# Kernel tuning notes

Measured on AMD Instinct MI355X. Metric: run time of the kernel, lower is better.

The kernel has to match this reference:

```python
import jax, jax.numpy as jnp
import numpy as np

B, CIN, COUT, H, W = 8, 28, 28, 256, 256
DG, KH, PADH = 7, 7, 3
CPG = CIN // DG  # channels per deformable group


def setup_inputs() -> dict:
    key = jax.random.key(0)
    ks = jax.random.split(key, 6)
    x = jax.random.normal(ks[0], (B, CIN, H, W), jnp.float32)
    weight = jax.random.normal(ks[1], (COUT, CIN, KH, 1), jnp.float32) * 0.02
    bias = jnp.zeros((COUT,), jnp.float32)
    w_t = jax.random.normal(ks[2], (COUT, COUT, 1, 7), jnp.float32) * 0.05
    b_t = jax.random.normal(ks[3], (COUT,), jnp.float32) * 0.05
    w_m = jax.random.normal(ks[4], (DG, DG, 1), jnp.float32) * 0.3
    b_m = jax.random.normal(ks[5], (DG,), jnp.float32) * 0.05
    return {"x": x, "weight": weight, "bias": bias,
            "w_t": w_t, "b_t": b_t, "w_m": w_m, "b_m": b_m}


def _sample_positions(height):
    # Faithful to init_offset: off[g, 2*i, h] = -i + (h+1)/(g+1)*(i+1) - (h+1)
    # x-offset channels stay 0, so sampling only moves along the H (frequency) axis.
    h = jnp.arange(height, dtype=jnp.float32)
    i = jnp.arange(KH, dtype=jnp.float32)
    g = jnp.arange(DG, dtype=jnp.float32)
    off = (-i[None, :, None]
           + (h[None, None, :] + 1.0) / (g[:, None, None] + 1.0) * (i[None, :, None] + 1.0)
           - (h[None, None, :] + 1.0))
    # DCNv2 sample row: h*stride - pad + i*dilation + offset_y
    return h[None, None, :] - PADH + i[None, :, None] + off  # (DG, KH, H)


def reference(x, weight, bias, w_t, b_t, w_m, b_m):
    yp = _sample_positions(H)                       # (DG, KH, H) float sample rows
    y0 = jnp.floor(yp)
    fy = yp - y0                                    # bilinear fraction along H
    y0i = y0.astype(jnp.int32)
    v0ok = ((y0i >= 0) & (y0i <= H - 1)).astype(x.dtype)
    v1ok = ((y0i + 1 >= 0) & (y0i + 1 <= H - 1)).astype(x.dtype)
    y0c = jnp.clip(y0i, 0, H - 1)
    y1c = jnp.clip(y0i + 1, 0, H - 1)

    x_r = x.reshape(B, DG, CPG, H, W)               # offsets grouped over channels
    g_b = jnp.broadcast_to(jnp.arange(DG)[:, None, None], (DG, KH, H))

    def gather(yi):
        v = x_r[:, g_b, :, yi, :]                   # (DG, KH, H, B, CPG, W)
        return jnp.transpose(v, (3, 0, 4, 1, 2, 5))  # (B, DG, CPG, KH, H, W)

    w0 = ((1.0 - fy) * v0ok)[None, :, None, :, :, None]
    w1 = (fy * v1ok)[None, :, None, :, :, None]
    sampled = gather(y0c) * w0 + gather(y1c) * w1   # mask is all-ones in HarmonicConv

    w_r = weight.reshape(COUT, DG, CPG, KH)         # (O, I, 7, 1) -> group view
    out = jnp.einsum('bgcihw,ogci->bohw', sampled, w_r) + bias[None, :, None, None]

    # temporal_conv: Conv2d(C, C, (1,7), pad (0,3))
    out = jax.lax.conv_general_dilated(
        out, w_t, (1, 1), ((0, 0), (3, 3)),
        dimension_numbers=('NCHW', 'OIHW', 'NCHW')) + b_t[None, :, None, None]

    # mixing_conv: Conv1d(7, 7, 1) over reshape (B, 7, C*H*W/7)
    sh = out.shape
    o = out.reshape(B, DG, -1)
    o = jnp.einsum('bgl,fg->bfl', o, w_m[:, :, 0]) + b_m[None, :, None]
    return o.reshape(sh)
```

## Files before the change

### kernel.cpp

```cpp
#include <hip/hip_runtime.h>
#include <hip/hip_bf16.h>

#define B_    8
#define CIN_  28
#define COUT_ 28
#define H_    256
#define W_    256
#define DG_   7
#define KH_   7
#define CPG_  4
#define HW_   (H_*W_)

typedef short short8 __attribute__((ext_vector_type(8)));
typedef short short4v __attribute__((ext_vector_type(4)));
typedef float f32x4 __attribute__((ext_vector_type(4)));

__device__ __forceinline__ short f2bf(float f) {
  __hip_bfloat16 h = __float2bfloat16(f);
  return *reinterpret_cast<short*>(&h);
}

__global__ void prep_weights(const float* __restrict__ weight, const float* __restrict__ bias,
                             const float* __restrict__ w_t, const float* __restrict__ b_t,
                             const float* __restrict__ w_m, const float* __restrict__ b_m,
                             short* __restrict__ A1, short* __restrict__ A2,
                             float* __restrict__ bias32, float* __restrict__ beff32) {
  int idx = blockIdx.x * blockDim.x + threadIdx.x;
  if (idx < 7168) {
    int j = idx & 7;
    int rest = idx >> 3;
    int l = rest & 63;
    int gm = rest >> 6;
    int g = gm % 7, mt = gm / 7;
    int o = mt * 16 + (l & 15);
    int kk = (l >> 4) * 8 + j;
    float v = 0.f;
    if (o < COUT_ && kk < 28) {
      int i = kk >> 2, c = kk & 3;
      v = weight[(o * CIN_ + (g * 4 + c)) * KH_ + i];
    }
    A1[idx] = f2bf(v);
  } else if (idx < 14336) {
    int id = idx - 7168;
    int j = id & 7;
    int rest = id >> 3;
    int l = rest & 63;
    int gm = rest >> 6;
    int ks = gm % 7, mt = gm / 7;
    int o = mt * 16 + (l & 15);
    int kk = (l >> 4) * 8 + j;
    float v = 0.f;
    if (o < COUT_ && kk < 28) {
      int f = o >> 2, cc = o & 3;
#pragma unroll
      for (int g = 0; g < DG_; ++g)
        v += w_m[f * 7 + g] * w_t[((g * 4 + cc) * COUT_ + kk) * 7 + ks];
    }
    A2[id] = f2bf(v);
  }
  if (idx < 32) {
    bias32[idx] = (idx < COUT_) ? bias[idx] : 0.f;
    float s = 0.f;
    if (idx < COUT_) {
      int f = idx >> 2, cc = idx & 3;
      s = b_m[f];
#pragma unroll
      for (int g = 0; g < DG_; ++g) s += w_m[f * 7 + g] * b_t[g * 4 + cc];
    }
    beff32[idx] = s;
  }
}

#define PITCH 40

__global__ __launch_bounds__(256)
void harmonic_mfma(const float* __restrict__ x,
                   const short* __restrict__ A1, const short* __restrict__ A2,
                   const float* __restrict__ bias32, const float* __restrict__ beff32,
                   float* __restrict__ out) {
  __shared__ short Bt[W_ * PITCH];
  __shared__ short Tt[(W_ + 6) * PITCH];

  const int bid = blockIdx.x;
  const int b = bid & 7;
  const int h = bid >> 3;
  const int tid = threadIdx.x;
  const int lane = tid & 63;
  const int wv = tid >> 6;
  const int l15 = lane & 15;
  const int l4 = lane >> 4;
  const int w = tid;

  if (tid < 96) {
    int rsel = tid >> 4;
    int r = (rsel < 3) ? rsel : (256 + rsel);
    ((int*)Tt)[r * (PITCH / 2) + (tid & 15)] = 0;
  }

  f32x4 acc[2][4] = {};
  const float* xb = x + (size_t)b * CIN_ * HW_ + w;

  for (int g = 0; g < DG_; ++g) {
#pragma unroll
    for (int i = 0; i < KH_; ++i) {
      float t   = ((float)(h + 1) / (float)(g + 1)) * (float)(i + 1);
      float off = ((float)(-i) + t) - (float)(h + 1);
      float yp  = (((float)h - 3.0f) + (float)i) + off;
      float y0f = floorf(yp);
      float fy  = yp - y0f;
      int y0i = (int)y0f;
      int y1i = y0i + 1;
      const bool ok0 = (y0i >= 0) && (y0i <= H_ - 1);
      const bool ok1 = (y1i >= 0) && (y1i <= H_ - 1);
      short4v pk = {0, 0, 0, 0};
      if (ok0 || ok1) {
        float a0 = ok0 ? (1.0f - fy) : 0.0f;
        float a1 = ok1 ? fy : 0.0f;
        int y0c = y0i < 0 ? 0 : (y0i > H_ - 1 ? H_ - 1 : y0i);
        int y1c = y1i < 0 ? 0 : (y1i > H_ - 1 ? H_ - 1 : y1i);
        const float* p0 = xb + (size_t)(g * CPG_) * HW_ + y0c * W_;
        const float* p1 = xb + (size_t)(g * CPG_) * HW_ + y1c * W_;
        float v0 = a0 * p0[0 * HW_] + a1 * p1[0 * HW_];
        float v1 = a0 * p0[1 * HW_] + a1 * p1[1 * HW_];
        float v2 = a0 * p0[2 * HW_] + a1 * p1[2 * HW_];
        float v3 = a0 * p0[3 * HW_] + a1 * p1[3 * HW_];
        pk = (short4v){f2bf(v0), f2bf(v1), f2bf(v2), f2bf(v3)};
      }
      *(short4v*)&Bt[w * PITCH + i * 4] = pk;
    }
    if (g == 0) *(short4v*)&Bt[w * PITCH + 28] = (short4v){0, 0, 0, 0};
    __syncthreads();

    short8 a0f = *(const short8*)&A1[((0 * 7 + g) * 64 + lane) * 8];
    short8 a1f = *(const short8*)&A1[((1 * 7 + g) * 64 + lane) * 8];
#pragma unroll
    for (int nt = 0; nt < 4; ++nt) {
      int wcol = wv * 64 + nt * 16 + l15;
      short8 bf = *(const short8*)&Bt[wcol * PITCH + l4 * 8];
      acc[0][nt] = __builtin_amdgcn_mfma_f32_16x16x32_bf16(a0f, bf, acc[0][nt], 0, 0, 0);
      acc[1][nt] = __builtin_amdgcn_mfma_f32_16x16x32_bf16(a1f, bf, acc[1][nt], 0, 0, 0);
    }
    __syncthreads();
  }

#pragma unroll
  for (int mt = 0; mt < 2; ++mt) {
#pragma unroll
    for (int nt = 0; nt < 4; ++nt) {
      int wcol = wv * 64 + nt * 16 + l15;
      int o0 = mt * 16 + l4 * 4;
      f32x4 v = acc[mt][nt];
      short4v pk = {f2bf(v[0] + bias32[o0 + 0]), f2bf(v[1] + bias32[o0 + 1]),
                    f2bf(v[2] + bias32[o0 + 2]), f2bf(v[3] + bias32[o0 + 3])};
      *(short4v*)&Tt[(wcol + 3) * PITCH + o0] = pk;
    }
  }
  __syncthreads();

  f32x4 acc2[2][4] = {};
#pragma unroll
  for (int ks = 0; ks < 7; ++ks) {
    short8 a20 = *(const short8*)&A2[((0 * 7 + ks) * 64 + lane) * 8];
    short8 a21 = *(const short8*)&A2[((1 * 7 + ks) * 64 + lane) * 8];
#pragma unroll
    for (int nt = 0; nt < 4; ++nt) {
      int wcol = wv * 64 + nt * 16 + l15;
      short8 bf = *(const short8*)&Tt[(wcol + ks) * PITCH + l4 * 8];
      acc2[0][nt] = __builtin_amdgcn_mfma_f32_16x16x32_bf16(a20, bf, acc2[0][nt], 0, 0, 0);
      acc2[1][nt] = __builtin_amdgcn_mfma_f32_16x16x32_bf16(a21, bf, acc2[1][nt], 0, 0, 0);
    }
  }

  float* ob = out + (size_t)b * COUT_ * HW_ + h * W_;
#pragma unroll
  for (int mt = 0; mt < 2; ++mt) {
#pragma unroll
    for (int nt = 0; nt < 4; ++nt) {
      int wcol = wv * 64 + nt * 16 + l15;
      int o0 = mt * 16 + l4 * 4;
      f32x4 v = acc2[mt][nt];
#pragma unroll
      for (int q = 0; q < 4; ++q) {
        int o = o0 + q;
        if (o < COUT_) ob[o * HW_ + wcol] = v[q] + beff32[o];
      }
    }
  }
}

extern "C" void kernel_launch(void* const* d_in, const int* in_sizes, int n_in,
                              void* d_out, int out_size, void* d_ws, size_t ws_size,
                              hipStream_t stream) {
  const float* x      = (const float*)d_in[0];
  const float* weight = (const float*)d_in[1];
  const float* bias   = (const float*)d_in[2];
  const float* w_t    = (const float*)d_in[3];
  const float* b_t    = (const float*)d_in[4];
  const float* w_m    = (const float*)d_in[5];
  const float* b_m    = (const float*)d_in[6];
  float* out = (float*)d_out;

  short* A1     = (short*)d_ws;
  short* A2     = A1 + 7168;
  float* bias32 = (float*)(A2 + 7168);
  float* beff32 = bias32 + 32;

  prep_weights<<<56, 256, 0, stream>>>(weight, bias, w_t, b_t, w_m, b_m,
                                       A1, A2, bias32, beff32);
  harmonic_mfma<<<B_ * H_, 256, 0, stream>>>(x, A1, A2, bias32, beff32, out);
}
```

Before: 181.7 us.

## Drop per-group block barriers, precompute tap table, and merge LDS buffers

Each wave now reads back only the LDS columns it wrote itself, so the two __syncthreads per deformable group are removed and the stage-1 tile is synchronised only once. Sample-row indices and bilinear weights are computed once per block into a small per-wave LDS table, instead of being recomputed in the unrolled tap loop. The two staging buffers are merged into one shared array, which roughly halves LDS use and may allow more resident blocks per CU. Stage-1 LDS writes are packed into wider 16-byte stores. The risk is that correctness now depends on wave-local LDS ordering and on reusing the merged buffer safely after the barrier.

```diff
diff --git a/kernel.cpp b/kernel.cpp
--- a/kernel.cpp
+++ b/kernel.cpp
@@ -10,14 +10,23 @@
 #define KH_   7
 #define CPG_  4
 #define HW_   (H_*W_)
-
-typedef short short8 __attribute__((ext_vector_type(8)));
+#define PITCH 40
+#define NTAP  (DG_*KH_)
+
+typedef short short8  __attribute__((ext_vector_type(8)));
 typedef short short4v __attribute__((ext_vector_type(4)));
-typedef float f32x4 __attribute__((ext_vector_type(4)));
+typedef float f32x4   __attribute__((ext_vector_type(4)));
 
 __device__ __forceinline__ short f2bf(float f) {
   __hip_bfloat16 h = __float2bfloat16(f);
   return *reinterpret_cast<short*>(&h);
+}
+
+__device__ __forceinline__ short8 cat8(short4v a, short4v b) {
+  short8 r;
+  r[0]=a[0]; r[1]=a[1]; r[2]=a[2]; r[3]=a[3];
+  r[4]=b[0]; r[5]=b[1]; r[6]=b[2]; r[7]=b[3];
+  return r;
 }
 
 __global__ void prep_weights(const float* __restrict__ weight, const float* __restrict__ bias,
@@ -71,15 +80,13 @@
   }
 }
 
-#define PITCH 40
-
 __global__ __launch_bounds__(256)
 void harmonic_mfma(const float* __restrict__ x,
                    const short* __restrict__ A1, const short* __restrict__ A2,
                    const float* __restrict__ bias32, const float* __restrict__ beff32,
                    float* __restrict__ out) {
-  __shared__ short Bt[W_ * PITCH];
-  __shared__ short Tt[(W_ + 6) * PITCH];
+  __shared__ short S[(W_ + 6) * PITCH];
+  __shared__ float4 yts[4][NTAP];
 
   const int bid = blockIdx.x;
   const int b = bid & 7;
@@ -91,56 +98,73 @@
   const int l4 = lane >> 4;
   const int w = tid;
 
+  if (lane < NTAP) {
+    int g = lane / 7;
+    int i = lane - g * 7;
+    float t   = ((float)(h + 1) / (float)(g + 1)) * (float)(i + 1);
+    float off = ((float)(-i) + t) - (float)(h + 1);
+    float yp  = (((float)h - 3.0f) + (float)i) + off;
+    float y0f = floorf(yp);
+    float fy  = yp - y0f;
+    int y0i = (int)y0f;
+    int y1i = y0i + 1;
+    bool ok0 = (y0i >= 0) && (y0i <= H_ - 1);
+    bool ok1 = (y1i >= 0) && (y1i <= H_ - 1);
+    float a0 = ok0 ? (1.0f - fy) : 0.0f;
+    float a1 = ok1 ? fy : 0.0f;
+    int y0c = y0i < 0 ? 0 : (y0i > H_ - 1 ? H_ - 1 : y0i);
+    int y1c = y1i < 0 ? 0 : (y1i > H_ - 1 ? H_ - 1 : y1i);
+    float4 e;
+    e.x = a0; e.y = a1;
+    e.z = __int_as_float(g * CPG_ * HW_ + y0c * W_);
+    e.w = __int_as_float(g * CPG_ * HW_ + y1c * W_);
+    yts[wv][lane] = e;
+  }
+
+  f32x4 acc[2][4] = {};
+  const float* xb = x + (size_t)b * CIN_ * HW_ + w;
+
+  *(short4v*)&S[w * PITCH + 28] = (short4v){0, 0, 0, 0};
+
+  for (int g = 0; g < DG_; ++g) {
+    short4v pk[KH_];
+#pragma unroll
+    for (int i = 0; i < KH_; ++i) {
+      float4 e = yts[wv][g * 7 + i];
+      short4v p = {0, 0, 0, 0};
+      if (!(e.x == 0.f && e.y == 0.f)) {
+        const float* p0 = xb + __float_as_int(e.z);
+        const float* p1 = xb + __float_as_int(e.w);
+        float v0 = e.x * p0[0 * HW_] + e.y * p1[0 * HW_];
+        float v1 = e.x * p0[1 * HW_] + e.y * p1[1 * HW_];
+        float v2 = e.x * p0[2 * HW_] + e.y * p1[2 * HW_];
+        float v3 = e.x * p0[3 * HW_] + e.y * p1[3 * HW_];
+        p = (short4v){f2bf(v0), f2bf(v1), f2bf(v2), f2bf(v3)};
+      }
+      pk[i] = p;
+    }
+    *(short8*)&S[w * PITCH + 0]   = cat8(pk[0], pk[1]);
+    *(short8*)&S[w * PITCH + 8]   = cat8(pk[2], pk[3]);
+    *(short8*)&S[w * PITCH + 16]  = cat8(pk[4], pk[5]);
+    *(short4v*)&S[w * PITCH + 24] = pk[6];
+
+    short8 a0f = *(const short8*)&A1[((0 * 7 + g) * 64 + lane) * 8];
+    short8 a1f = *(const short8*)&A1[((1 * 7 + g) * 64 + lane) * 8];
+#pragma unroll
+    for (int nt = 0; nt < 4; ++nt) {
+      int wcol = wv * 64 + nt * 16 + l15;
+      short8 bf = *(const short8*)&S[wcol * PITCH + l4 * 8];
+      acc[0][nt] = __builtin_amdgcn_mfma_f32_16x16x32_bf16(a0f, bf, acc[0][nt], 0, 0, 0);
+      acc[1][nt] = __builtin_amdgcn_mfma_f32_16x16x32_bf16(a1f, bf, acc[1][nt], 0, 0, 0);
+    }
+  }
+
+  __syncthreads();
+
   if (tid < 96) {
     int rsel = tid >> 4;
     int r = (rsel < 3) ? rsel : (256 + rsel);
-    ((int*)Tt)[r * (PITCH / 2) + (tid & 15)] = 0;
-  }
-
-  f32x4 acc[2][4] = {};
-  const float* xb = x + (size_t)b * CIN_ * HW_ + w;
-
-  for (int g = 0; g < DG_; ++g) {
-#pragma unroll
-    for (int i = 0; i < KH_; ++i) {
-      float t   = ((float)(h + 1) / (float)(g + 1)) * (float)(i + 1);
-      float off = ((float)(-i) + t) - (float)(h + 1);
-      float yp  = (((float)h - 3.0f) + (float)i) + off;
-      float y0f = floorf(yp);
-      float fy  = yp - y0f;
-      int y0i = (int)y0f;
-      int y1i = y0i + 1;
-      const bool ok0 = (y0i >= 0) && (y0i <= H_ - 1);
-      const bool ok1 = (y1i >= 0) && (y1i <= H_ - 1);
-      short4v pk = {0, 0, 0, 0};
-      if (ok0 || ok1) {
-        float a0 = ok0 ? (1.0f - fy) : 0.0f;
-        float a1 = ok1 ? fy : 0.0f;
-        int y0c = y0i < 0 ? 0 : (y0i > H_ - 1 ? H_ - 1 : y0i);
-        int y1c = y1i < 0 ? 0 : (y1i > H_ - 1 ? H_ - 1 : y1i);
-        const float* p0 = xb + (size_t)(g * CPG_) * HW_ + y0c * W_;
-        const float* p1 = xb + (size_t)(g * CPG_) * HW_ + y1c * W_;
-        float v0 = a0 * p0[0 * HW_] + a1 * p1[0 * HW_];
-        float v1 = a0 * p0[1 * HW_] + a1 * p1[1 * HW_];
-        float v2 = a0 * p0[2 * HW_] + a1 * p1[2 * HW_];
-        float v3 = a0 * p0[3 * HW_] + a1 * p1[3 * HW_];
-        pk = (short4v){f2bf(v0), f2bf(v1), f2bf(v2), f2bf(v3)};
-      }
-      *(short4v*)&Bt[w * PITCH + i * 4] = pk;
-    }
-    if (g == 0) *(short4v*)&Bt[w * PITCH + 28] = (short4v){0, 0, 0, 0};
-    __syncthreads();
-
-    short8 a0f = *(const short8*)&A1[((0 * 7 + g) * 64 + lane) * 8];
-    short8 a1f = *(const short8*)&A1[((1 * 7 + g) * 64 + lane) * 8];
-#pragma unroll
-    for (int nt = 0; nt < 4; ++nt) {
-      int wcol = wv * 64 + nt * 16 + l15;
-      short8 bf = *(const short8*)&Bt[wcol * PITCH + l4 * 8];
-      acc[0][nt] = __builtin_amdgcn_mfma_f32_16x16x32_bf16(a0f, bf, acc[0][nt], 0, 0, 0);
-      acc[1][nt] = __builtin_amdgcn_mfma_f32_16x16x32_bf16(a1f, bf, acc[1][nt], 0, 0, 0);
-    }
-    __syncthreads();
+    ((int*)S)[r * (PITCH / 2) + (tid & 15)] = 0;
   }
 
 #pragma unroll
@@ -152,7 +176,7 @@
       f32x4 v = acc[mt][nt];
       short4v pk = {f2bf(v[0] + bias32[o0 + 0]), f2bf(v[1] + bias32[o0 + 1]),
                     f2bf(v[2] + bias32[o0 + 2]), f2bf(v[3] + bias32[o0 + 3])};
-      *(short4v*)&Tt[(wcol + 3) * PITCH + o0] = pk;
+      *(short4v*)&S[(wcol + 3) * PITCH + o0] = pk;
     }
   }
   __syncthreads();
@@ -165,7 +189,7 @@
 #pragma unroll
     for (int nt = 0; nt < 4; ++nt) {
       int wcol = wv * 64 + nt * 16 + l15;
-      short8 bf = *(const short8*)&Tt[(wcol + ks) * PITCH + l4 * 8];
+      short8 bf = *(const short8*)&S[(wcol + ks) * PITCH + l4 * 8];
       acc2[0][nt] = __builtin_amdgcn_mfma_f32_16x16x32_bf16(a20, bf, acc2[0][nt], 0, 0, 0);
       acc2[1][nt] = __builtin_amdgcn_mfma_f32_16x16x32_bf16(a21, bf, acc2[1][nt], 0, 0, 0);
     }
```

After: 165.6 us. 1.1x faster.
